# Kernel optimization log

Hardware: AMD Instinct MI355X
Metric: run time of the kernel (lower is better)

The kernel has to match this reference:

```python
import jax, jax.numpy as jnp
import numpy as np
from functools import partial

# FCOSPostProcessor config (from __init__ defaults / hard-coded forward constants)
PRE_NMS_THRESH = 0.05
PRE_NMS_TOP_N = 1000
ML_NMS_THRESH = 0.6       # self.nms_thresh used in select_over_all_levels
FPN_POST_NMS_TOP_N = 100
SCORE_THRESH = 0.5        # hard-coded in forward
FINAL_NMS_THRESH = 0.9    # hard-coded in forward
NUM_CLASSES = 17          # 16 foreground logit channels

_STRIDES = (8, 16, 32, 64, 128)
_FEAT_HW = ((100, 160), (50, 80), (25, 40), (13, 20), (7, 10))
_BATCH = 8
_C = NUM_CLASSES - 1


def setup_inputs() -> dict:
    key = jax.random.key(0)
    inp = {}
    for lvl, (s, (h, w)) in enumerate(zip(_STRIDES, _FEAT_HW)):
        k1, k2, k3 = jax.random.split(jax.random.fold_in(key, lvl), 3)
        ys = jnp.arange(h, dtype=jnp.float32) * s + s // 2
        xs = jnp.arange(w, dtype=jnp.float32) * s + s // 2
        yy, xx = jnp.meshgrid(ys, xs, indexing='ij')
        inp[f'locations_{lvl}'] = jnp.stack([xx.reshape(-1), yy.reshape(-1)], axis=-1)  # (h*w, 2) xy
        inp[f'box_cls_{lvl}'] = jax.random.normal(k1, (_BATCH, _C, h, w), jnp.float32) * 2.0 - 5.0
        inp[f'box_regression_{lvl}'] = jax.random.uniform(k2, (_BATCH, 4, h, w), jnp.float32) * (4.0 * s)
        inp[f'centerness_{lvl}'] = jax.random.normal(k3, (_BATCH, 1, h, w), jnp.float32)
    inp['image_sizes'] = jnp.tile(jnp.array([[800, 1280]], jnp.int32), (_BATCH, 1))  # (h, w)
    return inp


def _decode_level(loc, cls, reg, ctr, image_sizes):
    # cls: (N,C,H,W) -> (N,HW,C) sigmoid; reg: (N,4,H,W) -> (N,HW,4); ctr: (N,1,H,W) -> (N,HW)
    N, C, H, W = cls.shape
    cls_s = jax.nn.sigmoid(jnp.transpose(cls, (0, 2, 3, 1)).reshape(N, H * W, C))
    reg_r = jnp.transpose(reg, (0, 2, 3, 1)).reshape(N, H * W, 4)
    ctr_s = jax.nn.sigmoid(ctr.reshape(N, H * W))
    cand = (cls_s > PRE_NMS_THRESH).reshape(N, -1)          # candidate mask (N, HW*C)
    sc = (cls_s * ctr_s[:, :, None]).reshape(N, -1)         # cls * centerness
    masked = jnp.where(cand, sc, -1.0)
    top_s, top_i = jax.lax.top_k(masked, PRE_NMS_TOP_N)     # padded top-k over threshold survivors
    valid = jnp.take_along_axis(cand, top_i, axis=1)
    loc_i = top_i // C
    labels = (top_i % C + 1).astype(jnp.int32)              # per_class = idx + 1
    pl = loc[loc_i]                                         # (N,K,2)
    idx4 = jnp.broadcast_to(loc_i[:, :, None], loc_i.shape + (4,))
    pr = jnp.take_along_axis(reg_r, idx4, axis=1)           # (N,K,4)
    x1 = pl[..., 0] - pr[..., 0]
    y1 = pl[..., 1] - pr[..., 1]
    x2 = pl[..., 0] + pr[..., 2]
    y2 = pl[..., 1] + pr[..., 3]
    # clip_to_image (TO_REMOVE = 1)
    hmax = (image_sizes[:, 0] - 1).astype(x1.dtype)[:, None]
    wmax = (image_sizes[:, 1] - 1).astype(x1.dtype)[:, None]
    boxes = jnp.stack([jnp.clip(x1, 0.0, wmax), jnp.clip(y1, 0.0, hmax),
                       jnp.clip(x2, 0.0, wmax), jnp.clip(y2, 0.0, hmax)], axis=-1)
    scores = jnp.where(valid, jnp.sqrt(jnp.maximum(top_s, 1e-12)), 0.0)  # sqrt(cls*ctr)
    return boxes, scores, labels, valid


def _iou(a, b):
    area_a = jnp.maximum(a[:, 2] - a[:, 0], 0.0) * jnp.maximum(a[:, 3] - a[:, 1], 0.0)
    area_b = jnp.maximum(b[:, 2] - b[:, 0], 0.0) * jnp.maximum(b[:, 3] - b[:, 1], 0.0)
    lt = jnp.maximum(a[:, None, :2], b[None, :, :2])
    rb = jnp.minimum(a[:, None, 2:], b[None, :, 2:])
    wh = jnp.maximum(rb - lt, 0.0)
    inter = wh[..., 0] * wh[..., 1]
    return inter / jnp.maximum(area_a[:, None] + area_b[None, :] - inter, 1e-9)


def _greedy_keep(boxes, scores, valid, thresh):
    # fixed-size greedy NMS on a single image; selection is discrete -> stop_gradient
    boxes = jax.lax.stop_gradient(boxes)
    scores = jax.lax.stop_gradient(scores)
    K = scores.shape[0]
    order = jnp.argsort(-jnp.where(valid, scores, -1.0))
    b = boxes[order]
    v = valid[order]
    iou = _iou(b, b)
    idx = jnp.arange(K)
    def body(i, keep):
        sup = (iou[i] > thresh) & keep[i] & (idx > i)
        return keep & (~sup)
    keep = jax.lax.fori_loop(0, K, body, v)
    return jnp.zeros(K, bool).at[order].set(keep)


def _pipeline(locs, clss, regs, ctrs, image_sizes):
    parts = [_decode_level(l, c, r, t, image_sizes)
             for l, c, r, t in zip(locs, clss, regs, ctrs)]
    boxes = jnp.concatenate([p[0] for p in parts], axis=1)   # (N, 5K, 4)
    scores = jnp.concatenate([p[1] for p in parts], axis=1)
    labels = jnp.concatenate([p[2] for p in parts], axis=1)
    valid = jnp.concatenate([p[3] for p in parts], axis=1)
    # multi-class NMS (boxlist_ml_nms): offset boxes per class so classes never overlap
    off = labels.astype(boxes.dtype) * (jax.lax.stop_gradient(jnp.max(boxes)) + 1.0)
    keep = jax.vmap(partial(_greedy_keep, thresh=ML_NMS_THRESH))(boxes + off[..., None], scores, valid)
    valid = valid & keep
    # fpn_post_nms_top_n cap (kthvalue-threshold in torch ~= top-k by score)
    _, idx = jax.lax.top_k(jnp.where(valid, scores, -1.0), FPN_POST_NMS_TOP_N)
    boxes = jnp.take_along_axis(boxes, jnp.broadcast_to(idx[:, :, None], idx.shape + (4,)), axis=1)
    scores = jnp.take_along_axis(scores, idx, axis=1)
    labels = jnp.take_along_axis(labels, idx, axis=1)
    valid = jnp.take_along_axis(valid, idx, axis=1)
    # choose_confident_boxes(score_thresh=0.5)
    valid = valid & (scores > SCORE_THRESH)
    # final class-agnostic boxlist_nms(0.9)
    keep2 = jax.vmap(partial(_greedy_keep, thresh=FINAL_NMS_THRESH))(boxes, scores, valid)
    valid = valid & keep2
    return (jnp.where(valid[..., None], boxes, 0.0),
            jnp.where(valid, scores, 0.0),
            jnp.where(valid, labels, 0),
            valid)


def reference(locations_0, locations_1, locations_2, locations_3, locations_4,
              box_cls_0, box_cls_1, box_cls_2, box_cls_3, box_cls_4,
              box_regression_0, box_regression_1, box_regression_2, box_regression_3, box_regression_4,
              centerness_0, centerness_1, centerness_2, centerness_3, centerness_4,
              image_sizes):
    locs = (locations_0, locations_1, locations_2, locations_3, locations_4)
    clss = (box_cls_0, box_cls_1, box_cls_2, box_cls_3, box_cls_4)
    regs = (box_regression_0, box_regression_1, box_regression_2, box_regression_3, box_regression_4)
    ctrs = (centerness_0, centerness_1, centerness_2, centerness_3, centerness_4)
    return _pipeline(locs, clss, regs, ctrs, image_sizes)
```

## Files before the change

kernel.cpp:

```cpp
#include <hip/hip_runtime.h>

#pragma clang fp contract(off)

typedef unsigned int u32;
typedef unsigned long long u64;
typedef unsigned char u8;

#define NIMG 8
#define NCLS 16
#define KSEL 1000
#define KIMG 5000
#define TOPN 100
#define CAP 576
#define NWRD 9
#define TIECAP 128
#define EPI 341280
#define HCH 4096
#define HBLK 84
#define ECH 16384
#define EBLK 23

__device__ inline int lvl_of(int i) {
  return (i < 256000) ? 0 : (i < 320000) ? 1 : (i < 336000) ? 2 : (i < 340160) ? 3 : 4;
}
__device__ inline int c_hw(int l)   { return l==0?16000: l==1?4000: l==2?1000: l==3?260: 70; }
__device__ inline int c_eoff(int l) { return l==0?0: l==1?256000: l==2?320000: l==3?336000: l==4?340160: 341280; }
__device__ inline int c_e(int l)    { return l==0?256000: l==1?64000: l==2?16000: l==3?4160: 1120; }

__device__ inline void blk_map(int b, int& lvl, int& bb, int& start, int& end) {
  if (b < 16)      { lvl = 0; bb = b; }
  else if (b < 20) { lvl = 1; bb = b - 16; }
  else             { lvl = b - 18; bb = 0; }
  start = c_eoff(lvl) + bb*ECH;
  int e = c_eoff(lvl + 1);
  end = (start + ECH < e) ? (start + ECH) : e;
}

struct Ptrs {
  const float* loc[5];
  const float* cls[5];
  const float* reg[5];
  const float* ctr[5];
  const int*   imsz;
};

__device__ inline u64 lmask_lt(int lane) { return lane ? (~0ull >> (64 - lane)) : 0ull; }

__device__ inline float sigm(float x) { return 1.0f / (1.0f + expf(-x)); }

__device__ inline float score_cand(const Ptrs& P, int img, int lvl, int c, int hw, bool& cand) {
  int HW = c_hw(lvl);
  float s = sigm(P.cls[lvl][(img*NCLS + c)*HW + hw]);
  cand = s > 0.05f;
  float t = sigm(P.ctr[lvl][img*HW + hw]);
  return s * t;
}

__device__ inline void box_decode(const Ptrs& P, int img, int lvl, int hw,
                                  float& x1, float& y1, float& x2, float& y2) {
  int HW = c_hw(lvl);
  float px = P.loc[lvl][hw*2+0];
  float py = P.loc[lvl][hw*2+1];
  float rl = P.reg[lvl][(img*4+0)*HW + hw];
  float rt = P.reg[lvl][(img*4+1)*HW + hw];
  float rr = P.reg[lvl][(img*4+2)*HW + hw];
  float rb = P.reg[lvl][(img*4+3)*HW + hw];
  float wmax = (float)(P.imsz[img*2+1] - 1);
  float hmax = (float)(P.imsz[img*2+0] - 1);
  x1 = fminf(fmaxf(px - rl, 0.0f), wmax);
  y1 = fminf(fmaxf(py - rt, 0.0f), hmax);
  x2 = fminf(fmaxf(px + rr, 0.0f), wmax);
  y2 = fminf(fmaxf(py + rb, 0.0f), hmax);
}

struct Det { float x1, y1, x2, y2, raw; bool cand; };

__device__ inline Det decode(const Ptrs& P, int img, int lvl, int c, int hw) {
  Det d;
  d.raw = score_cand(P, img, lvl, c, hw, d.cand);
  box_decode(P, img, lvl, hw, d.x1, d.y1, d.x2, d.y2);
  return d;
}

__device__ inline float iou_ref(float ax1, float ay1, float ax2, float ay2,
                                float bx1, float by1, float bx2, float by2) {
  float areaA = fmaxf(ax2-ax1, 0.0f) * fmaxf(ay2-ay1, 0.0f);
  float areaB = fmaxf(bx2-bx1, 0.0f) * fmaxf(by2-by1, 0.0f);
  float wx = fmaxf(fminf(ax2,bx2) - fmaxf(ax1,bx1), 0.0f);
  float wy = fmaxf(fminf(ay2,by2) - fmaxf(ay1,by1), 0.0f);
  float inter = wx * wy;
  return inter / fmaxf(areaA + areaB - inter, 1e-9f);
}

__global__ void k_zero(u32* w, int n) {
  for (int i = blockIdx.x*blockDim.x + threadIdx.x; i < n; i += gridDim.x*blockDim.x) {
    u32 val = 0;
    int rel = i - 40960;
    if (rel >= 0 && rel < 320 && (rel & 7) == 2) val = KSEL;
    w[i] = val;
  }
}

__global__ __launch_bounds__(256) void k_hist(Ptrs P, u32* hist, const u32* state, int pass) {
  __shared__ u32 lh[2][1024];
  int img = blockIdx.y;
  int chunk = blockIdx.x * HCH;
  for (int b = threadIdx.x; b < 2048; b += 256) ((u32*)lh)[b] = 0;
  int lvl0 = lvl_of(chunk);
  int prob0 = img*5 + lvl0;
  bool straddle = (lvl0 < 4) && (chunk + HCH > c_eoff(lvl0+1));
  u32 m0 = state[prob0*8+0], p0 = state[prob0*8+1];
  u32 m1 = 0, p1 = 0;
  if (straddle) { m1 = state[(prob0+1)*8+0]; p1 = state[(prob0+1)*8+1]; }
  int shift = (pass == 0) ? 20 : ((pass == 1) ? 10 : 0);
  __syncthreads();
  for (int k = 0; k < 16; ++k) {
    int i = chunk + k*256 + threadIdx.x;
    if (i >= EPI) break;
    int lvl = lvl0 + ((straddle && i >= c_eoff(lvl0+1)) ? 1 : 0);
    int li = i - c_eoff(lvl);
    int HW = c_hw(lvl);
    int c = li / HW, hw = li - c*HW;
    bool cand; float raw = score_cand(P, img, lvl, c, hw, cand);
    if (!cand) continue;
    u32 bits = __float_as_uint(raw);
    int bank = lvl - lvl0;
    u32 msk = bank ? m1 : m0, pfx = bank ? p1 : p0;
    if ((bits & msk) != pfx) continue;
    atomicAdd(&lh[bank][(bits >> shift) & 0x3FFu], 1u);
  }
  __syncthreads();
  for (int b = threadIdx.x; b < 2048; b += 256) {
    u32 v = ((u32*)lh)[b];
    if (v) atomicAdd(&hist[(prob0 + (b >> 10))*1024 + (b & 1023)], v);
  }
}

__global__ __launch_bounds__(256) void k_scan(u32* hist, u32* state, int pass) {
  __shared__ u32 sfx[1024];
  __shared__ int sbin;
  int prob = blockIdx.x;
  u32* h = hist + prob*1024;
  int tid = threadIdx.x;
  for (int r = tid; r < 1024; r += 256) sfx[r] = h[1023 - r];
  __syncthreads();
  for (int b = tid; b < 1024; b += 256) h[b] = 0;
  if (tid == 0) sbin = -1;
  for (int d = 1; d < 1024; d <<= 1) {
    u32 v[4];
#pragma unroll
    for (int k = 0; k < 4; ++k) {
      int i = tid + k*256;
      v[k] = sfx[i] + ((i >= d) ? sfx[i - d] : 0u);
    }
    __syncthreads();
#pragma unroll
    for (int k = 0; k < 4; ++k) sfx[tid + k*256] = v[k];
    __syncthreads();
  }
  u32 need = state[prob*8+2];
  u32 allM = state[prob*8+3];
  if (!allM) {
#pragma unroll
    for (int k = 0; k < 4; ++k) {
      int b = tid + k*256;
      u32 sb  = sfx[1023 - b];
      u32 sb1 = (b == 1023) ? 0u : sfx[1022 - b];
      if (sb >= need && sb1 < need) sbin = b;
    }
  }
  __syncthreads();
  if (tid == 0 && !allM) {
    u32* st = state + prob*8;
    if (sbin < 0) {
      st[3] = 1; st[0] = 0xFFFFFFFFu; st[1] = 0xFFFFFFFFu;
    } else {
      int shift = (pass == 0) ? 20 : ((pass == 1) ? 10 : 0);
      u32 rem = need - ((sbin == 1023) ? 0u : sfx[1022 - sbin]);
      st[1] |= ((u32)sbin) << shift;
      st[0] |= 0x3FFu << shift;
      st[2] = rem;
      if (pass == 2) { st[4] = st[1]; st[5] = rem; }
    }
  }
}

__global__ __launch_bounds__(256) void k_count(Ptrs P, const u32* state, u32* blockCnt) {
  int lvl, bb, start, end;
  blk_map(blockIdx.x, lvl, bb, start, end);
  int img = blockIdx.y;
  int prob = img*5 + lvl;
  int HW = c_hw(lvl);
  const float* clsBase = P.cls[lvl] + (size_t)img*NCLS*HW;
  const float* ctrBase = P.ctr[lvl] + (size_t)img*HW;
  u32 allMode = state[prob*8+3];
  u32 tstar = state[prob*8+4];
  int cnt = 0;
  for (int r = 0; r < 16; ++r) {
    int i0 = start + r*1024 + threadIdx.x*4;
    if (i0 >= end) continue;
    int li = i0 - c_eoff(lvl);
    float4 cv;
    if (i0 + 4 <= end) cv = *reinterpret_cast<const float4*>(clsBase + li);
    else {
      cv.x = clsBase[li];
      cv.y = (i0+1 < end) ? clsBase[li+1] : 0.0f;
      cv.z = (i0+2 < end) ? clsBase[li+2] : 0.0f;
      cv.w = (i0+3 < end) ? clsBase[li+3] : 0.0f;
    }
#pragma unroll
    for (int e = 0; e < 4; ++e) {
      int i = i0 + e;
      if (i >= end) break;
      float s = sigm((&cv.x)[e]);
      if (!(s > 0.05f)) continue;
      int lie = li + e;
      int hw = lie % HW;
      float t = sigm(ctrBase[hw]);
      u32 bits = __float_as_uint(s * t);
      if (allMode || bits > tstar) ++cnt;
    }
  }
  for (int d = 32; d >= 1; d >>= 1) cnt += __shfl_xor(cnt, d);
  __shared__ int ws[4];
  if ((threadIdx.x & 63) == 0) ws[threadIdx.x >> 6] = cnt;
  __syncthreads();
  if (threadIdx.x == 0) blockCnt[prob*16 + bb] = (u32)(ws[0] + ws[1] + ws[2] + ws[3]);
}

__global__ void k_bscan(const u32* blockCnt, u32* bbase, u32* counter) {
  int p = threadIdx.x;
  if (p >= 40) return;
  int lvl = p % 5;
  int nb = (lvl == 0) ? 16 : (lvl == 1) ? 4 : 1;
  u32 run = 0;
  for (int b = 0; b < nb; ++b) { bbase[p*16 + b] = run; run += blockCnt[p*16 + b]; }
  counter[p] = run;
}

__global__ __launch_bounds__(256) void k_emit(Ptrs P, const u32* state, const u32* bbase,
                                              u32* tieCnt, u32* tieIdx,
                                              u32* sbits, float* ssqrt, u32* slabel,
                                              float* sbox, u32* gmax) {
  __shared__ u32 wcnt[2][4];
  int lvl, bb, start, end;
  blk_map(blockIdx.x, lvl, bb, start, end);
  int img = blockIdx.y;
  int prob = img*5 + lvl;
  int HW = c_hw(lvl);
  const float* clsBase = P.cls[lvl] + (size_t)img*NCLS*HW;
  const float* ctrBase = P.ctr[lvl] + (size_t)img*HW;
  u32 allMode = state[prob*8+3];
  u32 tstar = state[prob*8+4];
  int lane = threadIdx.x & 63, wv = threadIdx.x >> 6;
  u64 lt = lmask_lt(lane);
  int running = (int)bbase[prob*16 + bb];
  float wmax = 0.0f;
  for (int r = 0; r < 16; ++r) {
    int i0 = start + r*1024 + threadIdx.x*4;
    int li = i0 - c_eoff(lvl);
    bool w[4] = {false,false,false,false};
    u32 bits[4] = {0,0,0,0};
    if (i0 < end) {
      float4 cv;
      if (i0 + 4 <= end) cv = *reinterpret_cast<const float4*>(clsBase + li);
      else {
        cv.x = clsBase[li];
        cv.y = (i0+1 < end) ? clsBase[li+1] : 0.0f;
        cv.z = (i0+2 < end) ? clsBase[li+2] : 0.0f;
        cv.w = (i0+3 < end) ? clsBase[li+3] : 0.0f;
      }
#pragma unroll
      for (int e = 0; e < 4; ++e) {
        int i = i0 + e;
        if (i >= end) break;
        float s = sigm((&cv.x)[e]);
        if (!(s > 0.05f)) continue;
        int lie = li + e;
        int c = lie / HW, hw = lie - c*HW;
        float t = sigm(ctrBase[hw]);
        u32 bi = __float_as_uint(s * t);
        if (allMode || bi > tstar) { w[e] = true; bits[e] = bi; }
        else if (bi == tstar) {
          u32 ts = atomicAdd(&tieCnt[prob], 1u);
          if (ts < TIECAP) tieIdx[prob*TIECAP + ts] = (u32)(hw*NCLS + c);
        }
      }
    }
    u64 b0 = __ballot(w[0]), b1 = __ballot(w[1]), b2 = __ballot(w[2]), b3 = __ballot(w[3]);
    int wvTot = (int)(__popcll(b0) + __popcll(b1) + __popcll(b2) + __popcll(b3));
    if (lane == 0) wcnt[r & 1][wv] = (u32)wvTot;
    __syncthreads();
    int preWave = 0, blockTot = 0;
#pragma unroll
    for (int k = 0; k < 4; ++k) {
      int v = (int)wcnt[r & 1][k];
      if (k < wv) preWave += v;
      blockTot += v;
    }
    int before = (int)(__popcll(b0 & lt) + __popcll(b1 & lt) + __popcll(b2 & lt) + __popcll(b3 & lt));
    int myBase = running + preWave + before;
    int acc = 0;
#pragma unroll
    for (int e = 0; e < 4; ++e) {
      if (!w[e]) continue;
      int slot = myBase + acc; ++acc;
      if (slot < KSEL) {
        int lie = li + e;
        int c = lie / HW, hw = lie - c*HW;
        float raw = __uint_as_float(bits[e]);
        float x1, y1, x2, y2;
        box_decode(P, img, lvl, hw, x1, y1, x2, y2);
        int idx = img*KIMG + lvl*KSEL + slot;
        sbits[idx]  = bits[e];
        ssqrt[idx]  = sqrtf(fmaxf(raw, 1e-12f));
        slabel[idx] = (u32)(c + 1);
        sbox[idx*4+0] = x1; sbox[idx*4+1] = y1;
        sbox[idx*4+2] = x2; sbox[idx*4+3] = y2;
        wmax = fmaxf(wmax, fmaxf(fmaxf(x1, y1), fmaxf(x2, y2)));
      }
    }
    running += blockTot;
  }
  for (int d = 32; d >= 1; d >>= 1) wmax = fmaxf(wmax, __shfl_xor(wmax, d));
  if (lane == 0 && wmax > 0.0f) atomicMax(gmax, __float_as_uint(wmax));
}

__global__ void k_ties(Ptrs P, const u32* state, u32* counter, const u32* tieCnt, const u32* tieIdx,
                       u32* sbits, float* ssqrt, u32* slabel, float* sbox, u32* gmax) {
  __shared__ u32 a[TIECAP];
  int prob = blockIdx.x;
  const u32* st = state + prob*8;
  if (st[3]) return;
  if (threadIdx.x != 0) return;
  int tn = (tieCnt[prob] < (u32)TIECAP) ? (int)tieCnt[prob] : TIECAP;
  int need = (int)st[5];
  int take = need < tn ? need : tn;
  if (take <= 0) return;
  for (int k = 0; k < tn; ++k) a[k] = tieIdx[prob*TIECAP + k];
  for (int k = 1; k < tn; ++k) {
    u32 v = a[k]; int m = k - 1;
    while (m >= 0 && a[m] > v) { a[m+1] = a[m]; --m; }
    a[m+1] = v;
  }
  int img = prob/5, lvl = prob%5;
  u32 cnt = counter[prob];
  for (int k = 0; k < take && cnt < (u32)KSEL; ++k) {
    u32 e = a[k]; int hw = (int)(e >> 4), c = (int)(e & 15u);
    Det d = decode(P, img, lvl, c, hw);
    int idx = img*KIMG + lvl*KSEL + (int)cnt;
    sbits[idx]  = __float_as_uint(d.raw);
    ssqrt[idx]  = sqrtf(fmaxf(d.raw, 1e-12f));
    slabel[idx] = (u32)(c + 1);
    sbox[idx*4+0] = d.x1; sbox[idx*4+1] = d.y1;
    sbox[idx*4+2] = d.x2; sbox[idx*4+3] = d.y2;
    float m4 = fmaxf(fmaxf(d.x1, d.y1), fmaxf(d.x2, d.y2));
    atomicMax(gmax, __float_as_uint(m4));
    ++cnt;
  }
  counter[prob] = cnt;
}

__global__ void k_deficit(Ptrs P, const u32* counter, u32* gmax) {
  int prob = blockIdx.x;
  int cnt = (int)counter[prob];
  if (cnt >= KSEL) return;
  int deficit = KSEL - cnt;
  int img = prob/5, lvl = prob%5;
  int E = c_e(lvl);
  int HW = c_hw(lvl);
  const float* clsBase = P.cls[lvl] + (size_t)img*NCLS*HW;
  int lane = threadIdx.x;
  int found = 0;
  float wmax = 0.0f;
  for (int base = 0; base < E && found < deficit; base += 64) {
    int e = base + lane;
    bool nc = false;
    if (e < E) nc = !(sigm(clsBase[(e & 15)*HW + (e >> 4)]) > 0.05f);
    u64 m = __ballot(nc);
    int pos = found + (int)__popcll(m & lmask_lt(lane));
    if (nc && pos < deficit) {
      float x1, y1, x2, y2;
      box_decode(P, img, lvl, e >> 4, x1, y1, x2, y2);
      wmax = fmaxf(wmax, fmaxf(fmaxf(x1, y1), fmaxf(x2, y2)));
    }
    found += (int)__popcll(m);
  }
  for (int d = 32; d >= 1; d >>= 1) wmax = fmaxf(wmax, __shfl_xor(wmax, d));
  if (lane == 0 && wmax > 0.0f) atomicMax(gmax, __float_as_uint(wmax));
}

__global__ __launch_bounds__(512) void k_sortlvl(const u32* sbits, u64* lkey) {
  __shared__ u64 sk[1024];
  int prob = blockIdx.x;
  int img = prob/5, lvl = prob%5;
  int tid = threadIdx.x;
  for (int i = tid; i < 1024; i += 512) {
    u64 key = 0ull;
    if (i < KSEL) {
      int slot = lvl*KSEL + i;
      key = (((u64)sbits[img*KIMG + slot]) << 32) | (u32)(KIMG - slot);
    }
    sk[i] = key;
  }
  __syncthreads();
  for (int ksz = 2; ksz <= 1024; ksz <<= 1) {
    for (int j = ksz >> 1; j >= 1; j >>= 1) {
      for (int i = tid; i < 1024; i += 512) {
        int ixj = i ^ j;
        if (ixj > i) {
          bool desc = ((i & ksz) == 0);
          u64 a = sk[i], b = sk[ixj];
          if (desc ? (a < b) : (a > b)) { sk[i] = b; sk[ixj] = a; }
        }
      }
      __syncthreads();
    }
  }
  for (int i = tid; i < KSEL; i += 512) lkey[prob*KSEL + i] = sk[i];
}

__global__ __launch_bounds__(256) void k_merge(const u64* lkey, u64* skey) {
  __shared__ u64 ll[5][KSEL];
  int prob = blockIdx.x;
  int img = prob/5, lvl = prob%5;
  int tid = threadIdx.x;
  for (int i = tid; i < 5*KSEL; i += 256)
    ll[i/KSEL][i%KSEL] = lkey[img*KIMG + i];
  __syncthreads();
  for (int j = tid; j < KSEL; j += 256) {
    u64 key = ll[lvl][j];
    int rank = j;
#pragma unroll
    for (int l2 = 0; l2 < 5; ++l2) {
      if (l2 == lvl) continue;
      int lo = 0, hi = KSEL;
      while (lo < hi) {
        int mid = (lo + hi) >> 1;
        if (ll[l2][mid] > key) lo = mid + 1; else hi = mid;
      }
      rank += lo;
    }
    skey[img*KIMG + rank] = key;
  }
}

__device__ inline int key_slot(u64 key) { return KIMG - (int)(key & 0xFFFFFFFFu); }

__global__ __launch_bounds__(256) void k_nms(const u64* skey, const u32* slabel, const float* sbox,
                                             const u32* gmax, u8* keep) {
  __shared__ float4 sb[CAP];
  __shared__ u32 srank[CAP];
  __shared__ u64 bm[CAP][NWRD];
  __shared__ u32 wcnt[4];
  __shared__ u64 kw[NWRD];
  __shared__ int sn;
  int img = blockIdx.x >> 4;
  int cls = (blockIdx.x & 15) + 1;
  int tid = threadIdx.x;
  int lane = tid & 63;
  int wv = tid >> 6;
  float off = (float)cls * (__uint_as_float(*gmax) + 1.0f);
  if (tid == 0) sn = 0;
  __syncthreads();
  for (int base = 0; base < KIMG; base += 256) {
    int r = base + tid;
    bool v = false; int slot = 0;
    if (r < KIMG) {
      u64 key = skey[img*KIMG + r];
      slot = key_slot(key);
      if ((key >> 32) != 0) v = (slabel[img*KIMG + slot] == (u32)cls);
    }
    u64 m = __ballot(v);
    int wrank = (int)__popcll(m & lmask_lt(lane));
    if (lane == 0) wcnt[wv] = (u32)__popcll(m);
    __syncthreads();
    int pos = sn + wrank;
    for (int k = 0; k < 4; ++k) if (k < wv) pos += (int)wcnt[k];
    if (v && pos < CAP) {
      const float* b = &sbox[(img*KIMG + slot)*4];
      sb[pos] = make_float4(b[0]+off, b[1]+off, b[2]+off, b[3]+off);
      srank[pos] = (u32)r;
    }
    __syncthreads();
    if (tid == 0) sn += (int)(wcnt[0]+wcnt[1]+wcnt[2]+wcnt[3]);
    __syncthreads();
  }
  int n = sn; if (n > CAP) n = CAP;
  for (int i = tid; i < n; i += 256) {
    float4 bi = sb[i];
    u64 w[NWRD];
#pragma unroll
    for (int q = 0; q < NWRD; ++q) w[q] = 0;
    for (int j = i + 1; j < n; ++j) {
      float4 bj = sb[j];
      if (iou_ref(bj.x,bj.y,bj.z,bj.w, bi.x,bi.y,bi.z,bi.w) > 0.6f)
        w[j >> 6] |= (1ull << (j & 63));
    }
#pragma unroll
    for (int q = 0; q < NWRD; ++q) bm[i][q] = w[q];
  }
  __syncthreads();
  if (wv == 0) {
    u64 kp = 0;
    if (lane < NWRD) {
      int cnt = n - lane*64;
      kp = (cnt >= 64) ? ~0ull : (cnt > 0 ? ((1ull << cnt) - 1ull) : 0ull);
    }
    for (int i = 0; i < n; ++i) {
      u64 row = (lane < NWRD) ? bm[i][lane] : 0ull;
      u64 kow = __shfl(kp, i >> 6);
      if ((kow >> (i & 63)) & 1ull) kp &= ~row;
    }
    if (lane < NWRD) kw[lane] = kp;
  }
  __syncthreads();
  for (int j = tid; j < n; j += 256)
    keep[img*KIMG + (int)srank[j]] = (u8)((kw[j >> 6] >> (j & 63)) & 1ull);
}

__global__ __launch_bounds__(64) void k_final(const u64* skey, const u8* keep, const float* ssqrt,
                                              const u32* slabel, const float* sbox, float* out) {
  __shared__ float sc[TOPN];
  __shared__ u32 lb[TOPN];
  __shared__ float4 bx[TOPN];
  int img = blockIdx.x;
  int lane = threadIdx.x;
  int cnt = 0;
  for (int base = 0; base < KIMG && cnt < TOPN; base += 64) {
    int r = base + lane;
    bool v = false; int slot = 0;
    if (r < KIMG) {
      u64 key = skey[img*KIMG + r];
      slot = key_slot(key);
      v = ((key >> 32) != 0) && (keep[img*KIMG + r] != 0);
    }
    u64 m = __ballot(v);
    int pos = cnt + (int)__popcll(m & lmask_lt(lane));
    if (v && pos < TOPN) {
      int sidx = img*KIMG + slot;
      sc[pos] = ssqrt[sidx];
      lb[pos] = slabel[sidx];
      bx[pos] = make_float4(sbox[sidx*4+0], sbox[sidx*4+1], sbox[sidx*4+2], sbox[sidx*4+3]);
    }
    cnt += (int)__popcll(m);
  }
  int n2 = cnt < TOPN ? cnt : TOPN;
  __syncthreads();
  u32 sup = 0;
  for (int i = 0; i < n2; ++i) {
    int owner = i & 63, s = i >> 6;
    u32 om = __shfl(sup, owner);
    bool vi = sc[i] > 0.5f;
    if (!vi || ((om >> s) & 1u)) continue;
    float4 bi = bx[i];
#pragma unroll
    for (int k = 0; k < 2; ++k) {
      int j = lane + (k << 6);
      if (j > i && j < n2 && !((sup >> k) & 1u)) {
        float4 bj = bx[j];
        if (iou_ref(bj.x, bj.y, bj.z, bj.w, bi.x, bi.y, bi.z, bi.w) > 0.9f)
          sup |= (1u << k);
      }
    }
  }
#pragma unroll
  for (int k = 0; k < 2; ++k) {
    int j = lane + (k << 6);
    if (j < TOPN) {
      bool ok = (j < n2) && (sc[j] > 0.5f) && !((sup >> k) & 1u);
      float4 b = ok ? bx[j] : make_float4(0.f, 0.f, 0.f, 0.f);
      float s  = ok ? sc[j] : 0.0f;
      float lf = ok ? (float)lb[j] : 0.0f;
      float vf = ok ? 1.0f : 0.0f;
      int ob = img*TOPN + j;
      out[ob*4+0] = b.x; out[ob*4+1] = b.y; out[ob*4+2] = b.z; out[ob*4+3] = b.w;
      out[NIMG*TOPN*4 + ob] = s;
      out[NIMG*TOPN*5 + ob] = lf;
      out[NIMG*TOPN*6 + ob] = vf;
    }
  }
}

extern "C" void kernel_launch(void* const* d_in, const int* in_sizes, int n_in,
                              void* d_out, int out_size, void* d_ws, size_t ws_size,
                              hipStream_t stream) {
  Ptrs P;
  bool dictOrder = (n_in >= 21) && (in_sizes[1] == 2048000);
  if (dictOrder) {
    for (int l = 0; l < 5; ++l) {
      P.loc[l] = (const float*)d_in[4*l + 0];
      P.cls[l] = (const float*)d_in[4*l + 1];
      P.reg[l] = (const float*)d_in[4*l + 2];
      P.ctr[l] = (const float*)d_in[4*l + 3];
    }
    P.imsz = (const int*)d_in[20];
  } else {
    for (int l = 0; l < 5; ++l) {
      P.loc[l] = (const float*)d_in[l];
      P.cls[l] = (const float*)d_in[5 + l];
      P.reg[l] = (const float*)d_in[10 + l];
      P.ctr[l] = (const float*)d_in[15 + l];
    }
    P.imsz = (const int*)d_in[20];
  }

  char* w = (char*)d_ws;
  u32* hist    = (u32*)w;  w += 40*1024*4;
  u32* state   = (u32*)w;  w += 40*8*4;
  u32* tieCnt  = (u32*)w;  w += 40*4;
  u32* gmax    = (u32*)w;  w += 64;
  u32* sbits   = (u32*)w;  w += NIMG*KIMG*4;
  u8*  keep    = (u8*)w;   w += NIMG*KIMG;
  size_t zbytes = (size_t)(w - (char*)d_ws);
  u32* counter  = (u32*)w;  w += 40*4;
  u32* blockCnt = (u32*)w;  w += 40*16*4;
  u32* bbase    = (u32*)w;  w += 40*16*4;
  u32* tieIdx   = (u32*)w;  w += 40*TIECAP*4;
  float* ssqrt  = (float*)w; w += NIMG*KIMG*4;
  u32* slabel   = (u32*)w;  w += NIMG*KIMG*4;
  float* sbox   = (float*)w; w += NIMG*KIMG*16;
  u64* skey     = (u64*)w;  w += NIMG*KIMG*8;
  u64* lkey     = (u64*)w;  w += NIMG*KIMG*8;

  size_t used = (size_t)(w - (char*)d_ws);
  if (used > ws_size) return;
  int zwords = (int)(zbytes / 4);

  k_zero<<<96, 256, 0, stream>>>((u32*)d_ws, zwords);
  for (int pass = 0; pass < 3; ++pass) {
    k_hist<<<dim3(HBLK, NIMG), 256, 0, stream>>>(P, hist, state, pass);
    k_scan<<<40, 256, 0, stream>>>(hist, state, pass);
  }
  k_count<<<dim3(EBLK, NIMG), 256, 0, stream>>>(P, state, blockCnt);
  k_bscan<<<1, 64, 0, stream>>>(blockCnt, bbase, counter);
  k_emit<<<dim3(EBLK, NIMG), 256, 0, stream>>>(P, state, bbase, tieCnt, tieIdx,
                                               sbits, ssqrt, slabel, sbox, gmax);
  k_ties<<<40, 64, 0, stream>>>(P, state, counter, tieCnt, tieIdx,
                                sbits, ssqrt, slabel, sbox, gmax);
  k_deficit<<<40, 64, 0, stream>>>(P, counter, gmax);
  k_sortlvl<<<40, 512, 0, stream>>>(sbits, lkey);
  k_merge<<<40, 256, 0, stream>>>(lkey, skey);
  k_nms<<<NIMG*NCLS, 256, 0, stream>>>(skey, slabel, sbox, gmax, keep);
  k_final<<<NIMG, 64, 0, stream>>>(skey, keep, ssqrt, slabel, sbox, (float*)d_out);
}
```

Measured before the change: 459.5 us.

## Skip sigmoid for clearly rejected logits and pre-bucket boxes per class before NMS

Adds an early reject that skips the sigmoid for logits at or below -2.95, which can never pass the 0.05 threshold, in the scoring, counting, emit and deficit paths. It also replaces the per-class NMS prologue, where each of the 128 blocks scanned all 5000 sorted keys, with a k_gather kernel. That kernel buckets boxes by class once per image into compact global arrays, so NMS blocks only load their own candidates. The cost is one extra launch, an 8-block gather with 16 ballots per step, and extra workspace aliased with lkey.

```diff
diff --git a/kernel.cpp b/kernel.cpp
--- a/kernel.cpp
+++ b/kernel.cpp
@@ -5,6 +5,7 @@
 typedef unsigned int u32;
 typedef unsigned long long u64;
 typedef unsigned char u8;
+typedef unsigned short u16;
 
 #define NIMG 8
 #define NCLS 16
@@ -19,6 +20,7 @@
 #define HBLK 84
 #define ECH 16384
 #define EBLK 23
+#define REJX (-2.95f)
 
 __device__ inline int lvl_of(int i) {
   return (i < 256000) ? 0 : (i < 320000) ? 1 : (i < 336000) ? 2 : (i < 340160) ? 3 : 4;
@@ -50,8 +52,11 @@
 
 __device__ inline float score_cand(const Ptrs& P, int img, int lvl, int c, int hw, bool& cand) {
   int HW = c_hw(lvl);
-  float s = sigm(P.cls[lvl][(img*NCLS + c)*HW + hw]);
+  float x = P.cls[lvl][(img*NCLS + c)*HW + hw];
+  if (x <= REJX) { cand = false; return 0.0f; }
+  float s = sigm(x);
   cand = s > 0.05f;
+  if (!cand) return 0.0f;
   float t = sigm(P.ctr[lvl][img*HW + hw]);
   return s * t;
 }
@@ -212,7 +217,9 @@
     for (int e = 0; e < 4; ++e) {
       int i = i0 + e;
       if (i >= end) break;
-      float s = sigm((&cv.x)[e]);
+      float x = (&cv.x)[e];
+      if (x <= REJX) continue;
+      float s = sigm(x);
       if (!(s > 0.05f)) continue;
       int lie = li + e;
       int hw = lie % HW;
@@ -274,7 +281,9 @@
       for (int e = 0; e < 4; ++e) {
         int i = i0 + e;
         if (i >= end) break;
-        float s = sigm((&cv.x)[e]);
+        float x = (&cv.x)[e];
+        if (x <= REJX) continue;
+        float s = sigm(x);
         if (!(s > 0.05f)) continue;
         int lie = li + e;
         int c = lie / HW, hw = lie - c*HW;
@@ -376,7 +385,10 @@
   for (int base = 0; base < E && found < deficit; base += 64) {
     int e = base + lane;
     bool nc = false;
-    if (e < E) nc = !(sigm(clsBase[(e & 15)*HW + (e >> 4)]) > 0.05f);
+    if (e < E) {
+      float x = clsBase[(e & 15)*HW + (e >> 4)];
+      nc = (x <= REJX) ? true : !(sigm(x) > 0.05f);
+    }
     u64 m = __ballot(nc);
     int pos = found + (int)__popcll(m & lmask_lt(lane));
     if (nc && pos < deficit) {
@@ -447,46 +459,75 @@
 
 __device__ inline int key_slot(u64 key) { return KIMG - (int)(key & 0xFFFFFFFFu); }
 
-__global__ __launch_bounds__(256) void k_nms(const u64* skey, const u32* slabel, const float* sbox,
-                                             const u32* gmax, u8* keep) {
-  __shared__ float4 sb[CAP];
-  __shared__ u32 srank[CAP];
-  __shared__ u64 bm[CAP][NWRD];
-  __shared__ u32 wcnt[4];
-  __shared__ u64 kw[NWRD];
-  __shared__ int sn;
-  int img = blockIdx.x >> 4;
-  int cls = (blockIdx.x & 15) + 1;
-  int tid = threadIdx.x;
-  int lane = tid & 63;
-  int wv = tid >> 6;
-  float off = (float)cls * (__uint_as_float(*gmax) + 1.0f);
-  if (tid == 0) sn = 0;
+__global__ __launch_bounds__(256) void k_gather(const u64* skey, const u32* slabel,
+                                                const float* sbox, const u32* gmax,
+                                                float* clsBox, u32* clsRank, u32* clsCnt) {
+  __shared__ u8  lbl[KIMG];
+  __shared__ u16 slt[KIMG];
+  __shared__ u16 pos[KIMG];
+  __shared__ u32 cnt[NCLS];
+  __shared__ u32 wtot[4][NCLS];
+  int img = blockIdx.x;
+  int tid = threadIdx.x, lane = tid & 63, wv = tid >> 6;
+  for (int r = tid; r < KIMG; r += 256) {
+    u64 key = skey[img*KIMG + r];
+    int slot = key_slot(key);
+    u8 c = 255;
+    if ((key >> 32) != 0) c = (u8)(slabel[img*KIMG + slot] - 1u);
+    lbl[r] = c;
+    slt[r] = (u16)slot;
+  }
+  if (tid < NCLS) cnt[tid] = 0;
   __syncthreads();
   for (int base = 0; base < KIMG; base += 256) {
     int r = base + tid;
-    bool v = false; int slot = 0;
-    if (r < KIMG) {
-      u64 key = skey[img*KIMG + r];
-      slot = key_slot(key);
-      if ((key >> 32) != 0) v = (slabel[img*KIMG + slot] == (u32)cls);
-    }
-    u64 m = __ballot(v);
-    int wrank = (int)__popcll(m & lmask_lt(lane));
-    if (lane == 0) wcnt[wv] = (u32)__popcll(m);
+    int c = (r < KIMG) ? (int)lbl[r] : 255;
+    u32 inWave = 0;
+#pragma unroll
+    for (int cc = 0; cc < NCLS; ++cc) {
+      u64 m = __ballot(c == cc);
+      if (c == cc) inWave = (u32)__popcll(m & lmask_lt(lane));
+      if (lane == 0) wtot[wv][cc] = (u32)__popcll(m);
+    }
     __syncthreads();
-    int pos = sn + wrank;
-    for (int k = 0; k < 4; ++k) if (k < wv) pos += (int)wcnt[k];
-    if (v && pos < CAP) {
-      const float* b = &sbox[(img*KIMG + slot)*4];
-      sb[pos] = make_float4(b[0]+off, b[1]+off, b[2]+off, b[3]+off);
-      srank[pos] = (u32)r;
+    if (r < KIMG && c != 255) {
+      u32 p = cnt[c] + inWave;
+      for (int k = 0; k < wv; ++k) p += wtot[k][c];
+      pos[r] = (u16)(p < 65535u ? p : 65535u);
     }
     __syncthreads();
-    if (tid == 0) sn += (int)(wcnt[0]+wcnt[1]+wcnt[2]+wcnt[3]);
+    if (tid < NCLS) cnt[tid] += wtot[0][tid] + wtot[1][tid] + wtot[2][tid] + wtot[3][tid];
     __syncthreads();
   }
-  int n = sn; if (n > CAP) n = CAP;
+  float goff = __uint_as_float(*gmax) + 1.0f;
+  for (int r = tid; r < KIMG; r += 256) {
+    int c = (int)lbl[r];
+    if (c == 255) continue;
+    u32 p = pos[r];
+    if (p >= CAP) continue;
+    int slot = (int)slt[r];
+    const float* b = &sbox[((size_t)img*KIMG + slot)*4];
+    float off = (float)(c + 1) * goff;
+    int o = (img*NCLS + c)*CAP + (int)p;
+    reinterpret_cast<float4*>(clsBox)[o] = make_float4(b[0]+off, b[1]+off, b[2]+off, b[3]+off);
+    clsRank[o] = (u32)r;
+  }
+  if (tid < NCLS) clsCnt[img*NCLS + tid] = cnt[tid];
+}
+
+__global__ __launch_bounds__(256) void k_nms(const float* clsBox, const u32* clsRank,
+                                             const u32* clsCnt, u8* keep) {
+  __shared__ float4 sb[CAP];
+  __shared__ u64 bm[CAP][NWRD];
+  __shared__ u64 kw[NWRD];
+  int img = blockIdx.x >> 4;
+  int cls = blockIdx.x & 15;
+  int pc = img*NCLS + cls;
+  int tid = threadIdx.x, lane = tid & 63, wv = tid >> 6;
+  int n = (int)clsCnt[pc]; if (n > CAP) n = CAP;
+  for (int j = tid; j < n; j += 256)
+    sb[j] = reinterpret_cast<const float4*>(clsBox)[pc*CAP + j];
+  __syncthreads();
   for (int i = tid; i < n; i += 256) {
     float4 bi = sb[i];
     u64 w[NWRD];
@@ -504,8 +545,8 @@
   if (wv == 0) {
     u64 kp = 0;
     if (lane < NWRD) {
-      int cnt = n - lane*64;
-      kp = (cnt >= 64) ? ~0ull : (cnt > 0 ? ((1ull << cnt) - 1ull) : 0ull);
+      int cnt2 = n - lane*64;
+      kp = (cnt2 >= 64) ? ~0ull : (cnt2 > 0 ? ((1ull << cnt2) - 1ull) : 0ull);
     }
     for (int i = 0; i < n; ++i) {
       u64 row = (lane < NWRD) ? bm[i][lane] : 0ull;
@@ -516,7 +557,7 @@
   }
   __syncthreads();
   for (int j = tid; j < n; j += 256)
-    keep[img*KIMG + (int)srank[j]] = (u8)((kw[j >> 6] >> (j & 63)) & 1ull);
+    keep[img*KIMG + (int)clsRank[pc*CAP + j]] = (u8)((kw[j >> 6] >> (j & 63)) & 1ull);
 }
 
 __global__ __launch_bounds__(64) void k_final(const u64* skey, const u8* keep, const float* ssqrt,
@@ -621,7 +662,10 @@
   u32* slabel   = (u32*)w;  w += NIMG*KIMG*4;
   float* sbox   = (float*)w; w += NIMG*KIMG*16;
   u64* skey     = (u64*)w;  w += NIMG*KIMG*8;
-  u64* lkey     = (u64*)w;  w += NIMG*KIMG*8;
+  float* clsBox = (float*)w; w += (size_t)NIMG*NCLS*CAP*16;
+  u32* clsRank  = (u32*)w;  w += (size_t)NIMG*NCLS*CAP*4;
+  u32* clsCnt   = (u32*)w;  w += NIMG*NCLS*4;
+  u64* lkey     = (u64*)clsBox;
 
   size_t used = (size_t)(w - (char*)d_ws);
   if (used > ws_size) return;
@@ -641,6 +685,7 @@
   k_deficit<<<40, 64, 0, stream>>>(P, counter, gmax);
   k_sortlvl<<<40, 512, 0, stream>>>(sbits, lkey);
   k_merge<<<40, 256, 0, stream>>>(lkey, skey);
-  k_nms<<<NIMG*NCLS, 256, 0, stream>>>(skey, slabel, sbox, gmax, keep);
+  k_gather<<<NIMG, 256, 0, stream>>>(skey, slabel, sbox, gmax, clsBox, clsRank, clsCnt);
+  k_nms<<<NIMG*NCLS, 256, 0, stream>>>(clsBox, clsRank, clsCnt, keep);
   k_final<<<NIMG, 64, 0, stream>>>(skey, keep, ssqrt, slabel, sbox, (float*)d_out);
 }
```

Result: slower. 484.9 us (+5.5%).
